# Kernel optimization log

Measured on AMD Instinct MI355X. Metric: run time of the kernel, lower is better.

Reference implementation:

```python
import jax, jax.numpy as jnp
import numpy as np

L, B, T, I, H, O = 2, 64, 256, 512, 1024, 256
HIDDEN_WEIGHT = 0.5  # placement_weight = 1 - hidden_weight
# dropout is identity in eval mode (reference is deterministic)


def setup_inputs() -> dict:
    key = jax.random.key(0)
    ks = jax.random.split(key, 20)
    def unif(k, shape, fan):
        b = 1.0 / np.sqrt(fan)
        return jax.random.uniform(k, shape, jnp.float32, -b, b)
    lengths = jax.random.randint(ks[4], (B,), 0, T + 1)
    lengths = lengths.at[0].set(T).at[1].set(0)  # exercise full-length and zero-length paths
    return {
        "step_input": jax.random.normal(ks[0], (B, T, I), jnp.float32),
        "clstm_hidden": jax.random.normal(ks[1], (B, H), jnp.float32),
        "hidden": jax.random.normal(ks[2], (L, B, H), jnp.float32),
        "cell": jax.random.normal(ks[3], (L, B, H), jnp.float32),
        "input_lengths": lengths.astype(jnp.int64),
        # LSTM params, PyTorch gate order [i, f, g, o]
        "w_ih0": unif(ks[5], (4 * H, I), H), "w_hh0": unif(ks[6], (4 * H, H), H),
        "b_ih0": unif(ks[7], (4 * H,), H), "b_hh0": unif(ks[8], (4 * H,), H),
        "w_ih1": unif(ks[9], (4 * H, H), H), "w_hh1": unif(ks[10], (4 * H, H), H),
        "b_ih1": unif(ks[11], (4 * H,), H), "b_hh1": unif(ks[12], (4 * H,), H),
        "w1": unif(ks[13], (H, H), H), "b1": unif(ks[14], (H,), H),
        "w2": unif(ks[15], (O, H), H), "b2": unif(ks[16], (O,), H),
    }


def compute_weighted_hidden(clstm_hidden, hidden, lens):
    # vectorized version of the per-(layer,batch) min-max rescale loop
    cmin = jnp.min(clstm_hidden, axis=-1, keepdims=True)            # [B,1]
    crange = jnp.max(clstm_hidden, axis=-1, keepdims=True) - cmin   # [B,1]
    safe_cr = jnp.where(crange > 0, crange, 1.0)
    s = jnp.where(crange > 0, (clstm_hidden - cmin) / safe_cr, clstm_hidden)  # [B,H]
    hmin = jnp.min(hidden, axis=-1, keepdims=True)                  # [L,B,1]
    hrange = jnp.max(hidden, axis=-1, keepdims=True) - hmin         # [L,B,1]
    s2 = jnp.where(hrange > 0, hmin + s[None] * hrange,
                   jnp.broadcast_to(s[None], hidden.shape))         # [L,B,H]
    c = jnp.where((lens == 0)[None, :, None], clstm_hidden[None], s2)
    return HIDDEN_WEIGHT * hidden + (1.0 - HIDDEN_WEIGHT) * c


def lstm_forward(x, h0, c0, lens, layer_params):
    # x: [B,T,I]; h0,c0: [L,B,H]; lens already clamped to >=1
    t_idx = jnp.arange(x.shape[1])

    def step(carry, xt_t):
        h, c = carry                      # each [L,B,H]
        xt, t = xt_t                      # xt: [B,I]
        valid = (t < lens)[:, None]       # [B,1]
        inp = xt
        hs, cs = [], []
        for l, (wih, whh, bih, bhh) in enumerate(layer_params):
            gates = inp @ wih.T + bih + h[l] @ whh.T + bhh   # [B,4H]
            i, f, g, o = jnp.split(gates, 4, axis=-1)
            i, f, o = jax.nn.sigmoid(i), jax.nn.sigmoid(f), jax.nn.sigmoid(o)
            g = jnp.tanh(g)
            c_new = f * c[l] + i * g
            h_new = o * jnp.tanh(c_new)
            hs.append(jnp.where(valid, h_new, h[l]))
            cs.append(jnp.where(valid, c_new, c[l]))
            inp = jnp.where(valid, h_new, 0.0)
        out_t = inp                        # top layer output, zeroed on padding
        return (jnp.stack(hs), jnp.stack(cs)), out_t

    (hn, cn), outs = jax.lax.scan(step, (h0, c0), (x.transpose(1, 0, 2), t_idx))
    return outs.transpose(1, 0, 2), hn, cn  # [B,T,H], [L,B,H], [L,B,H]


def reference(step_input, clstm_hidden, hidden, cell, input_lengths,
              w_ih0, w_hh0, b_ih0, b_hh0, w_ih1, w_hh1, b_ih1, b_hh1,
              w1, b1, w2, b2):
    weighted_hidden = compute_weighted_hidden(clstm_hidden, hidden, input_lengths)
    lens = jnp.clip(input_lengths, 1, None)  # torch.clamp(min=1)
    layer_params = [(w_ih0, w_hh0, b_ih0, b_hh0), (w_ih1, w_hh1, b_ih1, b_hh1)]
    lstm_out, hn, cn = lstm_forward(step_input, weighted_hidden, cell, lens, layer_params)
    # dropout layers are identity in eval mode
    h1 = jax.nn.relu(lstm_out @ w1.T + b1)
    logits = jax.nn.relu(h1 @ w2.T + b2)  # [B,T,O]
    zero = (input_lengths == 0)
    logits = jnp.where(zero[:, None, None], 0.0, logits)
    hn = jnp.where(zero[None, :, None], 0.0, hn)
    cn = jnp.where(zero[None, :, None], 0.0, cn)
    return logits, hn, cn
```

## Files before the change

### kernel.cpp

```cpp
#include <hip/hip_runtime.h>


typedef __bf16 bf16x8 __attribute__((ext_vector_type(8)));
typedef float f32x4 __attribute__((ext_vector_type(4)));
typedef int i32x4 __attribute__((ext_vector_type(4)));

__device__ __forceinline__ unsigned short f2bf(float f) {
  unsigned u = __float_as_uint(f);
  u = u + 0x7FFFu + ((u >> 16) & 1u);
  return (unsigned short)(u >> 16);
}
__device__ __forceinline__ float sigm_(float x) { return 1.f / (1.f + __expf(-x)); }
__device__ __forceinline__ float tanh_(float x) { return 1.f - 2.f / (__expf(2.f * x) + 1.f); }

__device__ __forceinline__ int hxoff(int b, int u) {
  return (b >> 4) * 16384 + (u >> 5) * 512 + ((u >> 3) & 3) * 128 + (b & 15) * 8 + (u & 7);
}

__global__ void cvt_kernel(const float* __restrict__ s, unsigned short* __restrict__ d, int n) {
  int i = (blockIdx.x * 256 + threadIdx.x) * 4;
  if (i < n) {
    float4 v = *reinterpret_cast<const float4*>(s + i);
    ushort4 o = make_ushort4(f2bf(v.x), f2bf(v.y), f2bf(v.z), f2bf(v.w));
    *reinterpret_cast<ushort4*>(d + i) = o;
  }
}

__global__ __launch_bounds__(256) void prep_kernel(
    const float* __restrict__ clstm, const float* __restrict__ hidden,
    const float* __restrict__ cell, const int* __restrict__ lens,
    float* __restrict__ hstate, float* __restrict__ cstate,
    unsigned short* __restrict__ h0buf, unsigned short* __restrict__ h1buf,
    const float* __restrict__ bih0, const float* __restrict__ bhh0,
    const float* __restrict__ bih1, const float* __restrict__ bhh1,
    float* __restrict__ bias0, float* __restrict__ bias1p,
    unsigned* __restrict__ bar) {
  const int tid = threadIdx.x, blk = blockIdx.x;
  const int l = blk >> 6, b = blk & 63;
  const float* crow = clstm + b * 1024;
  const float* hrow = hidden + ((size_t)l * 64 + b) * 1024;
  float cmn = 3.4e38f, cmx = -3.4e38f, hmn = 3.4e38f, hmx = -3.4e38f;
  for (int i = tid; i < 1024; i += 256) {
    float c = crow[i], h = hrow[i];
    cmn = fminf(cmn, c); cmx = fmaxf(cmx, c);
    hmn = fminf(hmn, h); hmx = fmaxf(hmx, h);
  }
#pragma unroll
  for (int off = 32; off > 0; off >>= 1) {
    cmn = fminf(cmn, __shfl_xor(cmn, off));
    cmx = fmaxf(cmx, __shfl_xor(cmx, off));
    hmn = fminf(hmn, __shfl_xor(hmn, off));
    hmx = fmaxf(hmx, __shfl_xor(hmx, off));
  }
  __shared__ float red[4][4];
  int wv = tid >> 6;
  if ((tid & 63) == 0) { red[wv][0] = cmn; red[wv][1] = cmx; red[wv][2] = hmn; red[wv][3] = hmx; }
  __syncthreads();
  cmn = fminf(fminf(red[0][0], red[1][0]), fminf(red[2][0], red[3][0]));
  cmx = fmaxf(fmaxf(red[0][1], red[1][1]), fmaxf(red[2][1], red[3][1]));
  hmn = fminf(fminf(red[0][2], red[1][2]), fminf(red[2][2], red[3][2]));
  hmx = fmaxf(fmaxf(red[0][3], red[1][3]), fmaxf(red[2][3], red[3][3]));
  const float crange = cmx - cmn, hrange = hmx - hmn;
  const int len = lens[b];
  const size_t base = ((size_t)l * 64 + b) * 1024;
  unsigned short* dst = (l == 0) ? h0buf : (h1buf + 65536);
  for (int i = tid; i < 1024; i += 256) {
    float cv = crow[i], hv = hrow[i];
    float s = (crange > 0.f) ? (cv - cmn) / crange : cv;
    float s2 = (hrange > 0.f) ? (hmn + s * hrange) : s;
    float cc = (len == 0) ? cv : s2;
    float w = 0.5f * hv + 0.5f * cc;
    hstate[base + i] = w;
    cstate[base + i] = cell[base + i];
    dst[hxoff(b, i)] = f2bf(w);
  }
  if (blk == 0) {
    for (int n = tid; n < 4096; n += 256) {
      bias0[n] = bih0[n] + bhh0[n];
      bias1p[(n & 1023) * 4 + (n >> 10)] = bih1[n] + bhh1[n];
      bar[n] = 0u;
    }
  }
}

template <int AMODE, int EPI>
__global__ __launch_bounds__(256) void gemm_kernel(
    const void* __restrict__ Ap, const unsigned short* __restrict__ Bw,
    void* __restrict__ Cout, const float* __restrict__ bias,
    const int* __restrict__ lens, int M, int N, int K, int t0) {
  __shared__ unsigned short Al[128][40];
  __shared__ unsigned short Bl[128][40];
  const int tid = threadIdx.x;
  const int m0 = blockIdx.y * 128, n0 = blockIdx.x * 128;
  const int srow = tid >> 2;
  const int c8 = (tid & 3) * 8;
  size_t aoff0, aoff1;
  {
    int r = m0 + srow, r2 = r + 64;
    if (AMODE == 0) {
      aoff0 = (size_t)r * K; aoff1 = (size_t)r2 * K;
    } else {
      aoff0 = ((size_t)(r & 63) * 256 + t0 + (r >> 6)) * K;
      aoff1 = ((size_t)(r2 & 63) * 256 + t0 + (r2 >> 6)) * K;
    }
  }
  const size_t boff0 = (size_t)(n0 + srow) * K, boff1 = (size_t)(n0 + srow + 64) * K;
  const int wave = tid >> 6, lane = tid & 63, ln = lane & 15, quad = lane >> 4;
  const int mq = (wave >> 1) * 64, nq = (wave & 1) * 64;
  f32x4 acc[4][4] = {};
  const int nkt = K >> 5;
  for (int kt = 0; kt < nkt; ++kt) {
    const int kc = kt * 32 + c8;
    if (AMODE == 1) {
      const float* A = (const float*)Ap;
      const float* p0 = A + aoff0 + kc;
      const float* p1 = A + aoff1 + kc;
      float4 v0 = *reinterpret_cast<const float4*>(p0);
      float4 v0b = *reinterpret_cast<const float4*>(p0 + 4);
      float4 v1 = *reinterpret_cast<const float4*>(p1);
      float4 v1b = *reinterpret_cast<const float4*>(p1 + 4);
      *reinterpret_cast<ushort4*>(&Al[srow][c8]) =
          make_ushort4(f2bf(v0.x), f2bf(v0.y), f2bf(v0.z), f2bf(v0.w));
      *reinterpret_cast<ushort4*>(&Al[srow][c8 + 4]) =
          make_ushort4(f2bf(v0b.x), f2bf(v0b.y), f2bf(v0b.z), f2bf(v0b.w));
      *reinterpret_cast<ushort4*>(&Al[srow + 64][c8]) =
          make_ushort4(f2bf(v1.x), f2bf(v1.y), f2bf(v1.z), f2bf(v1.w));
      *reinterpret_cast<ushort4*>(&Al[srow + 64][c8 + 4]) =
          make_ushort4(f2bf(v1b.x), f2bf(v1b.y), f2bf(v1b.z), f2bf(v1b.w));
    } else {
      const unsigned short* A = (const unsigned short*)Ap;
      *reinterpret_cast<int4*>(&Al[srow][c8]) = *reinterpret_cast<const int4*>(A + aoff0 + kc);
      *reinterpret_cast<int4*>(&Al[srow + 64][c8]) = *reinterpret_cast<const int4*>(A + aoff1 + kc);
    }
    *reinterpret_cast<int4*>(&Bl[srow][c8]) = *reinterpret_cast<const int4*>(Bw + boff0 + kc);
    *reinterpret_cast<int4*>(&Bl[srow + 64][c8]) = *reinterpret_cast<const int4*>(Bw + boff1 + kc);
    __syncthreads();
    bf16x8 af[4], bfr[4];
#pragma unroll
    for (int i = 0; i < 4; ++i) {
      af[i] = *reinterpret_cast<const bf16x8*>(&Al[mq + i * 16 + ln][quad * 8]);
      bfr[i] = *reinterpret_cast<const bf16x8*>(&Bl[nq + i * 16 + ln][quad * 8]);
    }
#pragma unroll
    for (int i = 0; i < 4; ++i)
#pragma unroll
      for (int j = 0; j < 4; ++j)
        acc[i][j] = __builtin_amdgcn_mfma_f32_16x16x32_bf16(af[i], bfr[j], acc[i][j], 0, 0, 0);
    __syncthreads();
  }
#pragma unroll
  for (int i = 0; i < 4; ++i) {
    int mmb = m0 + mq + i * 16 + quad * 4;
#pragma unroll
    for (int j = 0; j < 4; ++j) {
      int nn = n0 + nq + j * 16 + ln;
      float bv = bias[nn];
#pragma unroll
      for (int r = 0; r < 4; ++r) {
        int mm = mmb + r;
        float v = acc[i][j][r] + bv;
        if (EPI >= 1) v = fmaxf(v, 0.f);
        if (EPI == 2) {
          if (lens[mm >> 8] == 0) v = 0.f;
          ((float*)Cout)[(size_t)mm * N + nn] = v;
        } else if (EPI == 1) {
          ((unsigned short*)Cout)[(size_t)mm * N + nn] = f2bf(v);
        } else {
          size_t idx = ((size_t)mm * 128 + ((nn >> 3) & 127)) * 32 + (nn & 7) * 4 + (nn >> 10);
          ((float*)Cout)[idx] = v;
        }
      }
    }
  }
}

#define HLo(dst, ptr, off) \
  asm volatile("global_load_dwordx4 %0, %1, off offset:" off " sc0 sc1" \
               : "=v"(dst) : "v"(ptr))
#define HL4(h0, h1, h2, h3, ptr) \
  HLo(h0, ptr, "0"); HLo(h1, ptr, "1024"); HLo(h2, ptr, "2048"); HLo(h3, ptr, "3072")
#define HLF(dst, ptr) \
  asm volatile("global_load_dwordx4 %0, %1, off sc0 sc1" : "=v"(dst) : "v"(ptr))
#define HST(ptr, val) \
  asm volatile("global_store_dwordx4 %0, %1, off sc0 sc1" :: "v"(ptr), "v"(val) : "memory")

__global__ __launch_bounds__(512) void rec2_kernel(
    const unsigned short* __restrict__ whh0b,
    const unsigned short* __restrict__ wih1b,
    const unsigned short* __restrict__ whh1b,
    const float* __restrict__ G2,
    const float* __restrict__ bias1p,
    unsigned short* __restrict__ h0buf,
    unsigned short* __restrict__ h1buf,
    float* __restrict__ pre1buf,
    float* __restrict__ hstate, float* __restrict__ cstate,
    unsigned short* __restrict__ h1out,
    const int* __restrict__ lens, int t0, int nint, unsigned* __restrict__ bar,
    const float* __restrict__ xin,
    const unsigned short* __restrict__ wih0bk,
    float* __restrict__ Gnext,
    const float* __restrict__ bias0k,
    int t0n, int do_gemm) {
  __shared__ unsigned short wlds[32 * 1032];
  __shared__ float glds[2][64][73];
  __shared__ unsigned short hsh[64][16];
  __shared__ unsigned short Ag[2][128][40];
  __shared__ unsigned short Bg[2][128][40];
  const int tid = threadIdx.x;
  const int bid = blockIdx.x;

  if (bid >= 192) {
    if (!do_gemm) return;
    const int w = bid - 192;
    const int half = tid >> 8;
    const int tl = tid & 255;
    const int srow = tl >> 2;
    const int c8 = (tl & 3) * 8;
    const int wv = tl >> 6, lane2 = tl & 63, ln2 = lane2 & 15, qd = lane2 >> 4;
    const int mq = (wv >> 1) * 64, nq = (wv & 1) * 64;
    for (int it = 0; it < 8; ++it) {
      const int tau = it * 128 + w * 2 + half;
      const int m0 = (tau >> 5) * 128, n0 = (tau & 31) * 128;
      size_t aoff0, aoff1;
      {
        int r = m0 + srow, r2 = r + 64;
        aoff0 = ((size_t)(r & 63) * 256 + t0n + (r >> 6)) * 512;
        aoff1 = ((size_t)(r2 & 63) * 256 + t0n + (r2 >> 6)) * 512;
      }
      const size_t boff0 = (size_t)(n0 + srow) * 512;
      const size_t boff1 = (size_t)(n0 + srow + 64) * 512;
      f32x4 acc[4][4] = {};
#pragma unroll 1
      for (int kt = 0; kt < 16; ++kt) {
        const int kc = kt * 32 + c8;
        const float* p0 = xin + aoff0 + kc;
        const float* p1 = xin + aoff1 + kc;
        float4 v0 = *reinterpret_cast<const float4*>(p0);
        float4 v0b = *reinterpret_cast<const float4*>(p0 + 4);
        float4 v1 = *reinterpret_cast<const float4*>(p1);
        float4 v1b = *reinterpret_cast<const float4*>(p1 + 4);
        *reinterpret_cast<ushort4*>(&Ag[half][srow][c8]) =
            make_ushort4(f2bf(v0.x), f2bf(v0.y), f2bf(v0.z), f2bf(v0.w));
        *reinterpret_cast<ushort4*>(&Ag[half][srow][c8 + 4]) =
            make_ushort4(f2bf(v0b.x), f2bf(v0b.y), f2bf(v0b.z), f2bf(v0b.w));
        *reinterpret_cast<ushort4*>(&Ag[half][srow + 64][c8]) =
            make_ushort4(f2bf(v1.x), f2bf(v1.y), f2bf(v1.z), f2bf(v1.w));
        *reinterpret_cast<ushort4*>(&Ag[half][srow + 64][c8 + 4]) =
            make_ushort4(f2bf(v1b.x), f2bf(v1b.y), f2bf(v1b.z), f2bf(v1b.w));
        *reinterpret_cast<int4*>(&Bg[half][srow][c8]) =
            *reinterpret_cast<const int4*>(wih0bk + boff0 + kc);
        *reinterpret_cast<int4*>(&Bg[half][srow + 64][c8]) =
            *reinterpret_cast<const int4*>(wih0bk + boff1 + kc);
        __syncthreads();
        bf16x8 af[4], bfr[4];
#pragma unroll
        for (int i = 0; i < 4; ++i) {
          af[i] = *reinterpret_cast<const bf16x8*>(&Ag[half][mq + i * 16 + ln2][qd * 8]);
          bfr[i] = *reinterpret_cast<const bf16x8*>(&Bg[half][nq + i * 16 + ln2][qd * 8]);
        }
#pragma unroll
        for (int i = 0; i < 4; ++i)
#pragma unroll
          for (int j = 0; j < 4; ++j)
            acc[i][j] = __builtin_amdgcn_mfma_f32_16x16x32_bf16(af[i], bfr[j], acc[i][j], 0, 0, 0);
        __syncthreads();
      }
#pragma unroll
      for (int i = 0; i < 4; ++i) {
        int mmb = m0 + mq + i * 16 + qd * 4;
#pragma unroll
        for (int j = 0; j < 4; ++j) {
          int nn = n0 + nq + j * 16 + ln2;
          float bv = bias0k[nn];
#pragma unroll
          for (int r = 0; r < 4; ++r) {
            int mm = mmb + r;
            float v = acc[i][j][r] + bv;
            size_t idx = ((size_t)mm * 128 + ((nn >> 3) & 127)) * 32 + (nn & 7) * 4 + (nn >> 10);
            Gnext[idx] = v;
          }
        }
      }
    }
    return;
  }

  const bool isL1 = bid >= 128;
  const int g = bid & 127;
  {
    int r = tid >> 4;
    int c0 = (tid & 15) * 64;
    const unsigned short* src;
    if (!isL1)
      src = wih1b + (size_t)((r >> 3) * 1024 + g * 8 + (r & 7)) * 1024;
    else
      src = whh1b + (size_t)((2 + (r >> 4)) * 1024 + g * 16 + (r & 15)) * 1024;
    const i32x4* s4 = reinterpret_cast<const i32x4*>(src + c0);
    i32x4* dst = reinterpret_cast<i32x4*>(wlds + r * 1032 + c0);
#pragma unroll
    for (int j = 0; j < 8; ++j) dst[j] = s4[j];
  }
  const int wave = tid >> 6, lane = tid & 63, ln = lane & 15, quad = lane >> 4;
  const int mt = wave & 3, kw = wave >> 2;
  bf16x8 bregA[16], bregB[16];
  {
    const unsigned short *bpA, *bpB;
    if (!isL1) {
      bpA = whh0b + (size_t)((ln >> 3) * 1024 + g * 8 + (ln & 7)) * 1024 + kw * 512 + quad * 8;
      bpB = whh0b + (size_t)((2 + (ln >> 3)) * 1024 + g * 8 + (ln & 7)) * 1024 + kw * 512 + quad * 8;
    } else {
      bpA = whh1b + (size_t)(g * 16 + ln) * 1024 + kw * 512 + quad * 8;
      bpB = whh1b + (size_t)(1024 + g * 16 + ln) * 1024 + kw * 512 + quad * 8;
    }
#pragma unroll
    for (int kt = 0; kt < 16; ++kt) {
      bregA[kt] = *reinterpret_cast<const bf16x8*>(bpA + kt * 32);
      bregB[kt] = *reinterpret_cast<const bf16x8*>(bpB + kt * 32);
    }
  }
  const int b = tid >> 3, ul = tid & 7;
  const size_t sb0 = (size_t)(isL1 ? 65536 : 0) + (size_t)b * 1024 +
                     (isL1 ? g * 16 + ul : g * 8 + ul);
  float cm0 = cstate[sb0], hm0 = hstate[sb0];
  float cm1 = 0.f, hm1 = 0.f;
  if (isL1) { cm1 = cstate[sb0 + 8]; hm1 = hstate[sb0 + 8]; }
  int lv0 = lens[b];
  const int len = lv0 < 1 ? 1 : lv0;
  int lvA = lens[mt * 16 + ln];
  const int lenmA = lvA < 1 ? 1 : lvA;
  f32x4 b1a = {0.f, 0.f, 0.f, 0.f}, b1b = {0.f, 0.f, 0.f, 0.f};
  if (isL1) {
    b1a = *reinterpret_cast<const f32x4*>(bias1p + (g * 16 + ul) * 4);
    b1b = *reinterpret_cast<const f32x4*>(bias1p + (g * 16 + 8 + ul) * 4);
  }
  int lenp = 257;
  if (isL1 && tid < 128) { int lv = lens[tid >> 1]; lenp = lv < 1 ? 1 : lv; }
  const int puboff = (tid >> 4) * 16384 + (g >> 2) * 512 + (g & 3) * 128 + (tid & 15) * 8;
  const int pub1off = ((tid >> 1) >> 4) * 16384 + (g >> 1) * 512 +
                      ((g * 2 + (tid & 1)) & 3) * 128 + ((tid >> 1) & 15) * 8;
  const bf16x8 z8 = {};
  const i32x4 zi = {};
  __syncthreads();

  for (int k = 0; k < nint; ++k) {
    const int s = t0 + k;
    const bool actG = (!isL1) && (k < 64);
    const bool actP = (!isL1) && (s >= 1) && (s <= 256);
    const bool actL = isL1 && (s >= 2);
    if (actG || actP || actL) {
      f32x4 pga = {0.f, 0.f, 0.f, 0.f}, pgb = {0.f, 0.f, 0.f, 0.f};
      if (isL1) {
        const float* pr = pre1buf + (size_t)(s & 1) * 262144 +
                          ((size_t)b * 1024 + g * 16) * 4;
        HLF(pga, pr + ul * 4);
        HLF(pgb, pr + (8 + ul) * 4);
      }
      bf16x8 hf[16];
      const unsigned short* p = (isL1 ? h1buf + ((s - 1) & 1) * 65536
                                      : h0buf + (s & 1) * 65536) +
                                mt * 16384 + kw * 8192 + lane * 8;
      HL4(hf[0], hf[1], hf[2], hf[3], p);
      HL4(hf[4], hf[5], hf[6], hf[7], p + 2048);
      HL4(hf[8], hf[9], hf[10], hf[11], p + 4096);
      HL4(hf[12], hf[13], hf[14], hf[15], p + 6144);
      if (actG)
        pga = *reinterpret_cast<const f32x4*>(
            G2 + (((size_t)(k * 64 + b)) * 128 + g) * 32 + ul * 4);
      const bool maskA = (!isL1) && ((s - 1) >= lenmA);
      f32x4 acc0 = {0.f, 0.f, 0.f, 0.f}, acc1 = acc0, acc2 = acc0, acc3 = acc0;
      const unsigned short* wp = wlds + ln * 1032 + kw * 512 + quad * 8;
      asm volatile("s_waitcnt vmcnt(8)" ::: "memory");
      __builtin_amdgcn_sched_barrier(0);
#pragma unroll
      for (int kt = 0; kt < 8; ++kt) {
        const unsigned short* c = wp + kt * 32;
        bf16x8 bC = *reinterpret_cast<const bf16x8*>(c);
        bf16x8 bD = *reinterpret_cast<const bf16x8*>(c + 16512);
        bf16x8 a_ = hf[kt];
        acc0 = __builtin_amdgcn_mfma_f32_16x16x32_bf16(a_, bregA[kt], acc0, 0, 0, 0);
        acc1 = __builtin_amdgcn_mfma_f32_16x16x32_bf16(a_, bregB[kt], acc1, 0, 0, 0);
        bf16x8 am = maskA ? z8 : a_;
        acc2 = __builtin_amdgcn_mfma_f32_16x16x32_bf16(am, bC, acc2, 0, 0, 0);
        acc3 = __builtin_amdgcn_mfma_f32_16x16x32_bf16(am, bD, acc3, 0, 0, 0);
      }
      asm volatile("s_waitcnt vmcnt(0)" ::: "memory");
      __builtin_amdgcn_sched_barrier(0);
#pragma unroll
      for (int kt = 8; kt < 16; ++kt) {
        const unsigned short* c = wp + kt * 32;
        bf16x8 bC = *reinterpret_cast<const bf16x8*>(c);
        bf16x8 bD = *reinterpret_cast<const bf16x8*>(c + 16512);
        bf16x8 a_ = hf[kt];
        acc0 = __builtin_amdgcn_mfma_f32_16x16x32_bf16(a_, bregA[kt], acc0, 0, 0, 0);
        acc1 = __builtin_amdgcn_mfma_f32_16x16x32_bf16(a_, bregB[kt], acc1, 0, 0, 0);
        bf16x8 am = maskA ? z8 : a_;
        acc2 = __builtin_amdgcn_mfma_f32_16x16x32_bf16(am, bC, acc2, 0, 0, 0);
        acc3 = __builtin_amdgcn_mfma_f32_16x16x32_bf16(am, bD, acc3, 0, 0, 0);
      }
#pragma unroll
      for (int r = 0; r < 4; ++r) {
        float* gp = &glds[kw][mt * 16 + quad * 4 + r][0];
        gp[ln] = acc0[r]; gp[16 + ln] = acc1[r];
        gp[32 + ln] = acc2[r]; gp[48 + ln] = acc3[r];
      }
      __syncthreads();
      const float* g0 = &glds[0][b][0];
      const float* g1 = &glds[1][b][0];
      if (actG) {
        float pi = g0[ul] + g1[ul] + pga.x;
        float pf = g0[8 + ul] + g1[8 + ul] + pga.y;
        float pgg = g0[16 + ul] + g1[16 + ul] + pga.z;
        float po = g0[24 + ul] + g1[24 + ul] + pga.w;
        float ig = sigm_(pi), fg = sigm_(pf), gv = tanh_(pgg), og = sigm_(po);
        float cn_ = fg * cm0 + ig * gv;
        float hn_ = og * tanh_(cn_);
        if (s < len) { cm0 = cn_; hm0 = hn_; }
        hsh[b][ul] = f2bf(hm0);
      }
      if (actP) {
        f32x4 pv;
        pv.x = g0[32 + ul] + g1[32 + ul];
        pv.y = g0[40 + ul] + g1[40 + ul];
        pv.z = g0[48 + ul] + g1[48 + ul];
        pv.w = g0[56 + ul] + g1[56 + ul];
        float* pd = pre1buf + (size_t)((s - 1) & 1) * 262144 +
                    (size_t)b * 4096 + g * 32 + ul * 4;
        HST(pd, pv);
      }
      if (actL) {
        {
          float pi = g0[ul] + g1[ul] + pga.x + b1a.x;
          float pf = g0[16 + ul] + g1[16 + ul] + pga.y + b1a.y;
          float pgg = g0[32 + ul] + g1[32 + ul] + pga.z + b1a.z;
          float po = g0[48 + ul] + g1[48 + ul] + pga.w + b1a.w;
          float ig = sigm_(pi), fg = sigm_(pf), gv = tanh_(pgg), og = sigm_(po);
          float cn_ = fg * cm0 + ig * gv;
          float hn_ = og * tanh_(cn_);
          if (s - 2 < len) { cm0 = cn_; hm0 = hn_; }
          hsh[b][ul] = f2bf(hm0);
        }
        {
          int iu = 8 + ul;
          float pi = g0[iu] + g1[iu] + pgb.x + b1b.x;
          float pf = g0[16 + iu] + g1[16 + iu] + pgb.y + b1b.y;
          float pgg = g0[32 + iu] + g1[32 + iu] + pgb.z + b1b.z;
          float po = g0[48 + iu] + g1[48 + iu] + pgb.w + b1b.w;
          float ig = sigm_(pi), fg = sigm_(pf), gv = tanh_(pgg), og = sigm_(po);
          float cn_ = fg * cm1 + ig * gv;
          float hn_ = og * tanh_(cn_);
          if (s - 2 < len) { cm1 = cn_; hm1 = hn_; }
          hsh[b][iu] = f2bf(hm1);
        }
      }
      __syncthreads();
      if (!isL1) {
        if (actG && tid < 64) {
          i32x4 v = *reinterpret_cast<const i32x4*>(&hsh[tid][0]);
          unsigned short* d = h0buf + ((s + 1) & 1) * 65536 + puboff;
          HST(d, v);
        }
        asm volatile("s_waitcnt vmcnt(0)" ::: "memory");
      } else {
        if (tid < 128) {
          const int pb = tid >> 1, half = tid & 1;
          i32x4 v = *reinterpret_cast<const i32x4*>(&hsh[pb][half * 8]);
          unsigned short* d = h1buf + (s & 1) * 65536 + pub1off;
          HST(d, v);
          const int t = s - 2;
          i32x4 vo = (t < lenp) ? v : zi;
          *reinterpret_cast<i32x4*>(h1out + ((size_t)pb * 256 + t) * 1024 +
                                    g * 16 + half * 8) = vo;
          asm volatile("s_waitcnt vmcnt(1)" ::: "memory");
        }
      }
    }
    __syncthreads();
    if (tid == 0) {
      unsigned a = __hip_atomic_fetch_add(bar + ((bid >> 3) << 4), 1u,
                                          __ATOMIC_RELAXED, __HIP_MEMORY_SCOPE_AGENT);
      if ((a & 7u) == 7u) {
        const unsigned val = (unsigned)(s + 1);
        const int gi = bid >> 3;
#pragma unroll
        for (int rep = 0; rep < 8; ++rep)
          __hip_atomic_store(bar + 1024 + ((gi * 8 + rep) << 4), val,
                             __ATOMIC_RELAXED, __HIP_MEMORY_SCOPE_AGENT);
      }
    }
    if (tid < 24) {
      const unsigned tgt = (unsigned)(s + 1);
      while (__hip_atomic_load(bar + 1024 + ((tid * 8 + (bid & 7)) << 4),
                               __ATOMIC_RELAXED, __HIP_MEMORY_SCOPE_AGENT) < tgt)
        __builtin_amdgcn_s_sleep(2);
    }
    __syncthreads();
  }
  hstate[sb0] = hm0; cstate[sb0] = cm0;
  if (isL1) { hstate[sb0 + 8] = hm1; cstate[sb0 + 8] = cm1; }
}

__global__ void final_kernel(const float* __restrict__ hstate, const float* __restrict__ cstate,
                             const int* __restrict__ lens, float* __restrict__ out) {
  int i = blockIdx.x * 256 + threadIdx.x;
  int b = (i >> 10) & 63;
  float z = (lens[b] == 0) ? 0.f : 1.f;
  out[4194304 + i] = z * hstate[i];
  out[4325376 + i] = z * cstate[i];
}

extern "C" void kernel_launch(void* const* d_in, const int* in_sizes, int n_in,
                              void* d_out, int out_size, void* d_ws, size_t ws_size,
                              hipStream_t stream) {
  const float* x = (const float*)d_in[0];
  const float* clstm = (const float*)d_in[1];
  const float* hidden = (const float*)d_in[2];
  const float* cell = (const float*)d_in[3];
  const int* lens = (const int*)d_in[4];
  const float* wih0 = (const float*)d_in[5];
  const float* whh0 = (const float*)d_in[6];
  const float* bih0 = (const float*)d_in[7];
  const float* bhh0 = (const float*)d_in[8];
  const float* wih1 = (const float*)d_in[9];
  const float* whh1 = (const float*)d_in[10];
  const float* bih1 = (const float*)d_in[11];
  const float* bhh1 = (const float*)d_in[12];
  const float* w1 = (const float*)d_in[13];
  const float* b1 = (const float*)d_in[14];
  const float* w2 = (const float*)d_in[15];
  const float* b2 = (const float*)d_in[16];
  float* out = (float*)d_out;

  char* ws = (char*)d_ws;
  size_t off = 0;
  auto alloc = [&](size_t bytes) -> void* {
    void* p = ws + off;
    off += (bytes + 255) & ~(size_t)255;
    return p;
  };
  unsigned short* wih0_b = (unsigned short*)alloc(2097152ull * 2);
  unsigned short* whh0_b = (unsigned short*)alloc(4194304ull * 2);
  unsigned short* wih1_b = (unsigned short*)alloc(4194304ull * 2);
  unsigned short* whh1_b = (unsigned short*)alloc(4194304ull * 2);
  unsigned short* w1_b = (unsigned short*)alloc(1048576ull * 2);
  unsigned short* w2_b = (unsigned short*)alloc(262144ull * 2);
  float* bias0 = (float*)alloc(4096 * 4);
  float* bias1p = (float*)alloc(4096 * 4);
  float* hstate = (float*)alloc(131072ull * 4);
  float* cstate = (float*)alloc(131072ull * 4);
  unsigned short* h0buf = (unsigned short*)alloc(131072ull * 2);
  unsigned short* h1buf = (unsigned short*)alloc(131072ull * 2);
  float* pre1buf = (float*)alloc(524288ull * 4);
  unsigned* bar = (unsigned*)alloc(16384);
  float* G2a = (float*)alloc(16777216ull * 4);
  float* G2b = (float*)alloc(16777216ull * 4);
  unsigned short* h1out = (unsigned short*)alloc(16777216ull * 2);

  cvt_kernel<<<2048, 256, 0, stream>>>(wih0, wih0_b, 2097152);
  cvt_kernel<<<4096, 256, 0, stream>>>(whh0, whh0_b, 4194304);
  cvt_kernel<<<4096, 256, 0, stream>>>(wih1, wih1_b, 4194304);
  cvt_kernel<<<4096, 256, 0, stream>>>(whh1, whh1_b, 4194304);
  cvt_kernel<<<1024, 256, 0, stream>>>(w1, w1_b, 1048576);
  cvt_kernel<<<256, 256, 0, stream>>>(w2, w2_b, 262144);

  prep_kernel<<<128, 256, 0, stream>>>(clstm, hidden, cell, lens, hstate, cstate,
                                       h0buf, h1buf, bih0, bhh0, bih1, bhh1,
                                       bias0, bias1p, bar);

  gemm_kernel<1, 0><<<dim3(32, 32), 256, 0, stream>>>(x, wih0_b, G2a, bias0, lens,
                                                      4096, 4096, 512, 0);
  for (int c = 0; c < 4; ++c) {
    float* Gc = (c & 1) ? G2b : G2a;
    float* Gn = (c & 1) ? G2a : G2b;
    rec2_kernel<<<256, 512, 0, stream>>>(whh0_b, wih1_b, whh1_b, Gc, bias1p,
                                         h0buf, h1buf, pre1buf, hstate, cstate,
                                         h1out, lens, c * 64, (c == 3) ? 66 : 64, bar,
                                         x, wih0_b, Gn, bias0, (c + 1) * 64,
                                         (c < 3) ? 1 : 0);
  }
  gemm_kernel<0, 1><<<dim3(8, 128), 256, 0, stream>>>(h1out, w1_b, (void*)G2a, b1, lens,
                                                      16384, 1024, 1024, 0);
  gemm_kernel<0, 2><<<dim3(2, 128), 256, 0, stream>>>((const void*)G2a, w2_b, out, b2, lens,
                                                      16384, 256, 1024, 0);
  final_kernel<<<512, 256, 0, stream>>>(hstate, cstate, lens, out);
}
```

Baseline: 1.878 ms.

## Overlap half of the w1 projection GEMM with the final recurrence chunk

The idle spare blocks of the last recurrence launch now run the w1 GEMM, with ReLU and bf16 output, on the even 128-row tiles of h1out. The standalone w1 GEMM launch is halved to cover only the odd tiles through a t0 flag. The six weight-conversion launches are also merged into one kernel. Risk: the even tiles read h1out rows while the recurrence is still writing them, which needs a time/row ordering guarantee that the code does not obviously provide.

```diff
diff --git a/kernel.cpp b/kernel.cpp
--- a/kernel.cpp
+++ b/kernel.cpp
@@ -17,13 +17,25 @@
   return (b >> 4) * 16384 + (u >> 5) * 512 + ((u >> 3) & 3) * 128 + (b & 15) * 8 + (u & 7);
 }
 
-__global__ void cvt_kernel(const float* __restrict__ s, unsigned short* __restrict__ d, int n) {
-  int i = (blockIdx.x * 256 + threadIdx.x) * 4;
-  if (i < n) {
-    float4 v = *reinterpret_cast<const float4*>(s + i);
-    ushort4 o = make_ushort4(f2bf(v.x), f2bf(v.y), f2bf(v.z), f2bf(v.w));
-    *reinterpret_cast<ushort4*>(d + i) = o;
-  }
+__global__ void cvt6_kernel(
+    const float* __restrict__ wih0, const float* __restrict__ whh0,
+    const float* __restrict__ wih1, const float* __restrict__ whh1,
+    const float* __restrict__ w1, const float* __restrict__ w2,
+    unsigned short* __restrict__ wih0b, unsigned short* __restrict__ whh0b,
+    unsigned short* __restrict__ wih1b, unsigned short* __restrict__ whh1b,
+    unsigned short* __restrict__ w1b, unsigned short* __restrict__ w2b) {
+  size_t i = (size_t)(blockIdx.x * 256 + threadIdx.x) * 4;
+  const float* s; unsigned short* d; size_t off;
+  if (i < 2097152)       { s = wih0; d = wih0b; off = 0; }
+  else if (i < 6291456)  { s = whh0; d = whh0b; off = 2097152; }
+  else if (i < 10485760) { s = wih1; d = wih1b; off = 6291456; }
+  else if (i < 14680064) { s = whh1; d = whh1b; off = 10485760; }
+  else if (i < 15728640) { s = w1;   d = w1b;   off = 14680064; }
+  else                   { s = w2;   d = w2b;   off = 15728640; }
+  i -= off;
+  float4 v = *reinterpret_cast<const float4*>(s + i);
+  ushort4 o = make_ushort4(f2bf(v.x), f2bf(v.y), f2bf(v.z), f2bf(v.w));
+  *reinterpret_cast<ushort4*>(d + i) = o;
 }
 
 __global__ __launch_bounds__(256) void prep_kernel(
@@ -91,7 +103,9 @@
   __shared__ unsigned short Al[128][40];
   __shared__ unsigned short Bl[128][40];
   const int tid = threadIdx.x;
-  const int m0 = blockIdx.y * 128, n0 = blockIdx.x * 128;
+  const int m0 = (AMODE == 0 && EPI == 1 && t0 != 0) ? (blockIdx.y * 256 + 128)
+                                                     : blockIdx.y * 128;
+  const int n0 = blockIdx.x * 128;
   const int srow = tid >> 2;
   const int c8 = (tid & 3) * 8;
   size_t aoff0, aoff1;
@@ -197,10 +211,10 @@
     unsigned short* __restrict__ h1out,
     const int* __restrict__ lens, int t0, int nint, unsigned* __restrict__ bar,
     const float* __restrict__ xin,
-    const unsigned short* __restrict__ wih0bk,
+    const unsigned short* __restrict__ wemb,
     float* __restrict__ Gnext,
-    const float* __restrict__ bias0k,
-    int t0n, int do_gemm) {
+    const float* __restrict__ bemb,
+    int t0n, int gmode) {
   __shared__ unsigned short wlds[32 * 1032];
   __shared__ float glds[2][64][73];
   __shared__ unsigned short hsh[64][16];
@@ -210,7 +224,7 @@
   const int bid = blockIdx.x;
 
   if (bid >= 192) {
-    if (!do_gemm) return;
+    if (gmode == 0) return;
     const int w = bid - 192;
     const int half = tid >> 8;
     const int tl = tid & 255;
@@ -218,66 +232,119 @@
     const int c8 = (tl & 3) * 8;
     const int wv = tl >> 6, lane2 = tl & 63, ln2 = lane2 & 15, qd = lane2 >> 4;
     const int mq = (wv >> 1) * 64, nq = (wv & 1) * 64;
-    for (int it = 0; it < 8; ++it) {
-      const int tau = it * 128 + w * 2 + half;
-      const int m0 = (tau >> 5) * 128, n0 = (tau & 31) * 128;
-      size_t aoff0, aoff1;
-      {
-        int r = m0 + srow, r2 = r + 64;
-        aoff0 = ((size_t)(r & 63) * 256 + t0n + (r >> 6)) * 512;
-        aoff1 = ((size_t)(r2 & 63) * 256 + t0n + (r2 >> 6)) * 512;
-      }
-      const size_t boff0 = (size_t)(n0 + srow) * 512;
-      const size_t boff1 = (size_t)(n0 + srow + 64) * 512;
-      f32x4 acc[4][4] = {};
+    if (gmode == 1) {
+      for (int it = 0; it < 8; ++it) {
+        const int tau = it * 128 + w * 2 + half;
+        const int m0 = (tau >> 5) * 128, n0 = (tau & 31) * 128;
+        size_t aoff0, aoff1;
+        {
+          int r = m0 + srow, r2 = r + 64;
+          aoff0 = ((size_t)(r & 63) * 256 + t0n + (r >> 6)) * 512;
+          aoff1 = ((size_t)(r2 & 63) * 256 + t0n + (r2 >> 6)) * 512;
+        }
+        const size_t boff0 = (size_t)(n0 + srow) * 512;
+        const size_t boff1 = (size_t)(n0 + srow + 64) * 512;
+        f32x4 acc[4][4] = {};
 #pragma unroll 1
-      for (int kt = 0; kt < 16; ++kt) {
-        const int kc = kt * 32 + c8;
-        const float* p0 = xin + aoff0 + kc;
-        const float* p1 = xin + aoff1 + kc;
-        float4 v0 = *reinterpret_cast<const float4*>(p0);
-        float4 v0b = *reinterpret_cast<const float4*>(p0 + 4);
-        float4 v1 = *reinterpret_cast<const float4*>(p1);
-        float4 v1b = *reinterpret_cast<const float4*>(p1 + 4);
-        *reinterpret_cast<ushort4*>(&Ag[half][srow][c8]) =
-            make_ushort4(f2bf(v0.x), f2bf(v0.y), f2bf(v0.z), f2bf(v0.w));
-        *reinterpret_cast<ushort4*>(&Ag[half][srow][c8 + 4]) =
-            make_ushort4(f2bf(v0b.x), f2bf(v0b.y), f2bf(v0b.z), f2bf(v0b.w));
-        *reinterpret_cast<ushort4*>(&Ag[half][srow + 64][c8]) =
-            make_ushort4(f2bf(v1.x), f2bf(v1.y), f2bf(v1.z), f2bf(v1.w));
-        *reinterpret_cast<ushort4*>(&Ag[half][srow + 64][c8 + 4]) =
-            make_ushort4(f2bf(v1b.x), f2bf(v1b.y), f2bf(v1b.z), f2bf(v1b.w));
-        *reinterpret_cast<int4*>(&Bg[half][srow][c8]) =
-            *reinterpret_cast<const int4*>(wih0bk + boff0 + kc);
-        *reinterpret_cast<int4*>(&Bg[half][srow + 64][c8]) =
-            *reinterpret_cast<const int4*>(wih0bk + boff1 + kc);
-        __syncthreads();
-        bf16x8 af[4], bfr[4];
+        for (int kt = 0; kt < 16; ++kt) {
+          const int kc = kt * 32 + c8;
+          const float* p0 = xin + aoff0 + kc;
+          const float* p1 = xin + aoff1 + kc;
+          float4 v0 = *reinterpret_cast<const float4*>(p0);
+          float4 v0b = *reinterpret_cast<const float4*>(p0 + 4);
+          float4 v1 = *reinterpret_cast<const float4*>(p1);
+          float4 v1b = *reinterpret_cast<const float4*>(p1 + 4);
+          *reinterpret_cast<ushort4*>(&Ag[half][srow][c8]) =
+              make_ushort4(f2bf(v0.x), f2bf(v0.y), f2bf(v0.z), f2bf(v0.w));
+          *reinterpret_cast<ushort4*>(&Ag[half][srow][c8 + 4]) =
+              make_ushort4(f2bf(v0b.x), f2bf(v0b.y), f2bf(v0b.z), f2bf(v0b.w));
+          *reinterpret_cast<ushort4*>(&Ag[half][srow + 64][c8]) =
+              make_ushort4(f2bf(v1.x), f2bf(v1.y), f2bf(v1.z), f2bf(v1.w));
+          *reinterpret_cast<ushort4*>(&Ag[half][srow + 64][c8 + 4]) =
+              make_ushort4(f2bf(v1b.x), f2bf(v1b.y), f2bf(v1b.z), f2bf(v1b.w));
+          *reinterpret_cast<int4*>(&Bg[half][srow][c8]) =
+              *reinterpret_cast<const int4*>(wemb + boff0 + kc);
+          *reinterpret_cast<int4*>(&Bg[half][srow + 64][c8]) =
+              *reinterpret_cast<const int4*>(wemb + boff1 + kc);
+          __syncthreads();
+          bf16x8 af[4], bfr[4];
+#pragma unroll
+          for (int i = 0; i < 4; ++i) {
+            af[i] = *reinterpret_cast<const bf16x8*>(&Ag[half][mq + i * 16 + ln2][qd * 8]);
+            bfr[i] = *reinterpret_cast<const bf16x8*>(&Bg[half][nq + i * 16 + ln2][qd * 8]);
+          }
+#pragma unroll
+          for (int i = 0; i < 4; ++i)
+#pragma unroll
+            for (int j = 0; j < 4; ++j)
+              acc[i][j] = __builtin_amdgcn_mfma_f32_16x16x32_bf16(af[i], bfr[j], acc[i][j], 0, 0, 0);
+          __syncthreads();
+        }
 #pragma unroll
         for (int i = 0; i < 4; ++i) {
-          af[i] = *reinterpret_cast<const bf16x8*>(&Ag[half][mq + i * 16 + ln2][qd * 8]);
-          bfr[i] = *reinterpret_cast<const bf16x8*>(&Bg[half][nq + i * 16 + ln2][qd * 8]);
-        }
-#pragma unroll
-        for (int i = 0; i < 4; ++i)
-#pragma unroll
-          for (int j = 0; j < 4; ++j)
-            acc[i][j] = __builtin_amdgcn_mfma_f32_16x16x32_bf16(af[i], bfr[j], acc[i][j], 0, 0, 0);
-        __syncthreads();
-      }
-#pragma unroll
-      for (int i = 0; i < 4; ++i) {
-        int mmb = m0 + mq + i * 16 + qd * 4;
-#pragma unroll
-        for (int j = 0; j < 4; ++j) {
-          int nn = n0 + nq + j * 16 + ln2;
-          float bv = bias0k[nn];
-#pragma unroll
-          for (int r = 0; r < 4; ++r) {
-            int mm = mmb + r;
-            float v = acc[i][j][r] + bv;
-            size_t idx = ((size_t)mm * 128 + ((nn >> 3) & 127)) * 32 + (nn & 7) * 4 + (nn >> 10);
-            Gnext[idx] = v;
+          int mmb = m0 + mq + i * 16 + qd * 4;
+#pragma unroll
+          for (int j = 0; j < 4; ++j) {
+            int nn = n0 + nq + j * 16 + ln2;
+            float bv = bemb[nn];
+#pragma unroll
+            for (int r = 0; r < 4; ++r) {
+              int mm = mmb + r;
+              float v = acc[i][j][r] + bv;
+              size_t idx = ((size_t)mm * 128 + ((nn >> 3) & 127)) * 32 + (nn & 7) * 4 + (nn >> 10);
+              Gnext[idx] = v;
+            }
+          }
+        }
+      }
+    } else {
+      for (int it = 0; it < 4; ++it) {
+        const int tau = it * 128 + w * 2 + half;
+        const int m0 = (tau >> 3) * 256;
+        const int n0 = (tau & 7) * 128;
+        const size_t aoff0 = (size_t)(m0 + srow) * 1024;
+        const size_t aoff1 = (size_t)(m0 + srow + 64) * 1024;
+        const size_t boff0 = (size_t)(n0 + srow) * 1024;
+        const size_t boff1 = (size_t)(n0 + srow + 64) * 1024;
+        f32x4 acc[4][4] = {};
+#pragma unroll 1
+        for (int kt = 0; kt < 32; ++kt) {
+          const int kc = kt * 32 + c8;
+          *reinterpret_cast<int4*>(&Ag[half][srow][c8]) =
+              *reinterpret_cast<const int4*>(h1out + aoff0 + kc);
+          *reinterpret_cast<int4*>(&Ag[half][srow + 64][c8]) =
+              *reinterpret_cast<const int4*>(h1out + aoff1 + kc);
+          *reinterpret_cast<int4*>(&Bg[half][srow][c8]) =
+              *reinterpret_cast<const int4*>(wemb + boff0 + kc);
+          *reinterpret_cast<int4*>(&Bg[half][srow + 64][c8]) =
+              *reinterpret_cast<const int4*>(wemb + boff1 + kc);
+          __syncthreads();
+          bf16x8 af[4], bfr[4];
+#pragma unroll
+          for (int i = 0; i < 4; ++i) {
+            af[i] = *reinterpret_cast<const bf16x8*>(&Ag[half][mq + i * 16 + ln2][qd * 8]);
+            bfr[i] = *reinterpret_cast<const bf16x8*>(&Bg[half][nq + i * 16 + ln2][qd * 8]);
+          }
+#pragma unroll
+          for (int i = 0; i < 4; ++i)
+#pragma unroll
+            for (int j = 0; j < 4; ++j)
+              acc[i][j] = __builtin_amdgcn_mfma_f32_16x16x32_bf16(af[i], bfr[j], acc[i][j], 0, 0, 0);
+          __syncthreads();
+        }
+#pragma unroll
+        for (int i = 0; i < 4; ++i) {
+          int mmb = m0 + mq + i * 16 + qd * 4;
+#pragma unroll
+          for (int j = 0; j < 4; ++j) {
+            int nn = n0 + nq + j * 16 + ln2;
+            float bv = bemb[nn];
+#pragma unroll
+            for (int r = 0; r < 4; ++r) {
+              int mm = mmb + r;
+              float v = fmaxf(acc[i][j][r] + bv, 0.f);
+              ((unsigned short*)Gnext)[(size_t)mm * 1024 + nn] = f2bf(v);
+            }
           }
         }
       }
@@ -555,12 +622,8 @@
   float* G2b = (float*)alloc(16777216ull * 4);
   unsigned short* h1out = (unsigned short*)alloc(16777216ull * 2);
 
-  cvt_kernel<<<2048, 256, 0, stream>>>(wih0, wih0_b, 2097152);
-  cvt_kernel<<<4096, 256, 0, stream>>>(whh0, whh0_b, 4194304);
-  cvt_kernel<<<4096, 256, 0, stream>>>(wih1, wih1_b, 4194304);
-  cvt_kernel<<<4096, 256, 0, stream>>>(whh1, whh1_b, 4194304);
-  cvt_kernel<<<1024, 256, 0, stream>>>(w1, w1_b, 1048576);
-  cvt_kernel<<<256, 256, 0, stream>>>(w2, w2_b, 262144);
+  cvt6_kernel<<<15616, 256, 0, stream>>>(wih0, whh0, wih1, whh1, w1, w2,
+                                         wih0_b, whh0_b, wih1_b, whh1_b, w1_b, w2_b);
 
   prep_kernel<<<128, 256, 0, stream>>>(clstm, hidden, cell, lens, hstate, cstate,
                                        h0buf, h1buf, bih0, bhh0, bih1, bhh1,
@@ -571,14 +634,20 @@
   for (int c = 0; c < 4; ++c) {
     float* Gc = (c & 1) ? G2b : G2a;
     float* Gn = (c & 1) ? G2a : G2b;
-    rec2_kernel<<<256, 512, 0, stream>>>(whh0_b, wih1_b, whh1_b, Gc, bias1p,
-                                         h0buf, h1buf, pre1buf, hstate, cstate,
-                                         h1out, lens, c * 64, (c == 3) ? 66 : 64, bar,
-                                         x, wih0_b, Gn, bias0, (c + 1) * 64,
-                                         (c < 3) ? 1 : 0);
-  }
-  gemm_kernel<0, 1><<<dim3(8, 128), 256, 0, stream>>>(h1out, w1_b, (void*)G2a, b1, lens,
-                                                      16384, 1024, 1024, 0);
+    if (c < 3) {
+      rec2_kernel<<<256, 512, 0, stream>>>(whh0_b, wih1_b, whh1_b, Gc, bias1p,
+                                           h0buf, h1buf, pre1buf, hstate, cstate,
+                                           h1out, lens, c * 64, 64, bar,
+                                           x, wih0_b, Gn, bias0, (c + 1) * 64, 1);
+    } else {
+      rec2_kernel<<<256, 512, 0, stream>>>(whh0_b, wih1_b, whh1_b, Gc, bias1p,
+                                           h0buf, h1buf, pre1buf, hstate, cstate,
+                                           h1out, lens, c * 64, 66, bar,
+                                           x, w1_b, G2a, b1, 0, 2);
+    }
+  }
+  gemm_kernel<0, 1><<<dim3(8, 64), 256, 0, stream>>>(h1out, w1_b, (void*)G2a, b1, lens,
+                                                     16384, 1024, 1024, 1);
   gemm_kernel<0, 2><<<dim3(2, 128), 256, 0, stream>>>((const void*)G2a, w2_b, out, b2, lens,
                                                       16384, 256, 1024, 0);
   final_kernel<<<512, 256, 0, stream>>>(hstate, cstate, lens, out);
```

Result: faster. 1.831 ms (-2.5%).
